# Kernel optimization log

Measured on AMD Instinct MI355X. Metric: run time of the kernel, lower is better.

## Reference

```python
import jax, jax.numpy as jnp
import numpy as np

B, S, V, E = 64, 100, 20000, 128
U, I = 10000, 20000


def setup_inputs() -> dict:
    key = jax.random.key(0)
    ks = jax.random.split(key, 12)
    initrange = 0.1
    return {
        "attr_item": jax.random.randint(ks[0], (B, S), 0, V, dtype=jnp.int32),
        "attr_tf_item": jax.random.uniform(ks[1], (B, S), dtype=jnp.float32),
        "attr_lens_item": jax.random.randint(ks[2], (B,), 1, S + 1, dtype=jnp.int32),
        "item_ids": jax.random.randint(ks[3], (B,), 0, I, dtype=jnp.int32),
        "attr_user": jax.random.randint(ks[4], (B, S), 0, V, dtype=jnp.int32),
        "attr_tf_user": jax.random.uniform(ks[5], (B, S), dtype=jnp.float32),
        "attr_lens_user": jax.random.randint(ks[6], (B,), 1, S + 1, dtype=jnp.int32),
        "user_ids": jax.random.randint(ks[7], (B,), 0, U, dtype=jnp.int32),
        "W_item": jax.random.uniform(ks[8], (V, E), jnp.float32, -initrange, initrange),
        "W_user": jax.random.uniform(ks[9], (V, E), jnp.float32, -initrange, initrange),
        "user_emb": jax.random.uniform(ks[10], (U, E), jnp.float32, -initrange, initrange),
        "item_emb": jax.random.uniform(ks[11], (I, E), jnp.float32, -initrange, initrange),
    }


def _cluster_logits(attr_ids, attr_tf, attr_lens, W):
    # attr_ids: [B,S] int, attr_tf: [B,S] float, attr_lens: [B] int, W: [V,E]
    seq = attr_ids.shape[1]
    mask = (jnp.arange(seq)[None, :] < attr_lens[:, None]).astype(attr_tf.dtype)  # [B,S]
    emb = W[attr_ids]                                   # [B,S,E]
    scores = jnp.einsum("bse,ve->bsv", emb, W)          # [B,S,V]
    cw = jax.nn.softmax(scores, axis=1)                 # softmax over seq dim (dim=1 in torch)
    # Algebraically identical to the [B,S,V,E] broadcast-mul-sum in the original:
    # logits[b,v] = sum_s (tf*mask)[b,s] * cw[b,s,v] * scores[b,s,v]
    return jnp.einsum("bs,bsv,bsv->bv", attr_tf * mask, cw, scores)


def reference(attr_item, attr_tf_item, attr_lens_item, item_ids,
              attr_user, attr_tf_user, attr_lens_user, user_ids,
              W_item, W_user, user_emb, item_emb):
    logits = _cluster_logits(attr_item, attr_tf_item, attr_lens_item, W_item)
    logits = logits + _cluster_logits(attr_user, attr_tf_user, attr_lens_user, W_user)
    logits = logits + user_emb[user_ids] @ W_user.T     # [B,V]
    logits = logits + item_emb[item_ids] @ W_item.T     # [B,V]
    return logits
```

## Files before the change

kernel.cpp:

```cpp
#include <hip/hip_runtime.h>

#define VDIM 20000
#define EDIM 128
#define BATCH 64
#define SEQ 100

typedef float f32x4 __attribute__((ext_vector_type(4)));
typedef short bf16x8 __attribute__((ext_vector_type(8)));
typedef unsigned short ushortx8 __attribute__((ext_vector_type(8)));

typedef __attribute__((address_space(1))) const unsigned int gas_u32;
typedef __attribute__((address_space(3))) unsigned int las_u32;

__device__ __forceinline__ void async16(unsigned short* lds, const unsigned short* g) {
  __builtin_amdgcn_global_load_lds((gas_u32*)g, (las_u32*)lds, 16, 0, 0);
}

__device__ __forceinline__ unsigned short f2bf(float f) {
  unsigned u = __builtin_bit_cast(unsigned, f);
  u += 0x7FFFu + ((u >> 16) & 1u);
  return (unsigned short)(u >> 16);
}

__global__ void prep_kernel(const float* __restrict__ Wi, const float* __restrict__ Wu,
                            const int* __restrict__ attr_item, const int* __restrict__ attr_user,
                            const int* __restrict__ item_ids, const int* __restrict__ user_ids,
                            const float* __restrict__ item_emb, const float* __restrict__ user_emb,
                            unsigned short* __restrict__ wbf, unsigned short* __restrict__ abf) {
  const int bid = blockIdx.x, t = threadIdx.x;
  if (bid < 2500) {
    const int c = bid & 1;
    const float* src = c ? Wu : Wi;
    unsigned short* dst = wbf + (size_t)c * (VDIM * EDIM);
    const int i0 = ((bid >> 1) * 256 + t) * 8;
    float4 a = *(const float4*)(src + i0);
    float4 b = *(const float4*)(src + i0 + 4);
    ushortx8 o;
    o[0] = f2bf(a.x); o[1] = f2bf(a.y); o[2] = f2bf(a.z); o[3] = f2bf(a.w);
    o[4] = f2bf(b.x); o[5] = f2bf(b.y); o[6] = f2bf(b.z); o[7] = f2bf(b.w);
    *(ushortx8*)(dst + i0) = o;
  } else {
    const int g = bid - 2500;
    const int b = g & 63, c = g >> 6;
    const int r = t >> 1, h = t & 1;
    const int* ids = c ? attr_user : attr_item;
    const float* W = c ? Wu : Wi;
    const float* demb = c ? user_emb : item_emb;
    const int* dids = c ? user_ids : item_ids;
    unsigned short* dst = abf + (size_t)(c * BATCH + b) * 16384;
    const float* src = nullptr;
    if (r < SEQ)       src = W + (size_t)ids[b * SEQ + r] * EDIM;
    else if (r == SEQ) src = demb + (size_t)dids[b] * EDIM;
    if (src) {
      #pragma unroll
      for (int k = 0; k < 8; ++k) {
        const int jj = h * 8 + k;
        const int j = jj ^ (r & 15);
        float4 a  = *(const float4*)(src + j * 8);
        float4 bb = *(const float4*)(src + j * 8 + 4);
        ushortx8 o;
        o[0] = f2bf(a.x);  o[1] = f2bf(a.y);  o[2] = f2bf(a.z);  o[3] = f2bf(a.w);
        o[4] = f2bf(bb.x); o[5] = f2bf(bb.y); o[6] = f2bf(bb.z); o[7] = f2bf(bb.w);
        *(ushortx8*)(dst + (r * 16 + jj) * 8) = o;
      }
    } else {
      ushortx8 z = {0, 0, 0, 0, 0, 0, 0, 0};
      #pragma unroll
      for (int k = 0; k < 8; ++k) *(ushortx8*)(dst + (r * 16 + h * 8 + k) * 8) = z;
    }
  }
}

__global__ __launch_bounds__(256, 2)
void main_kernel(const unsigned short* __restrict__ wbf, const unsigned short* __restrict__ abf,
                 const float* __restrict__ tf_item, const int* __restrict__ lens_item,
                 const float* __restrict__ tf_user, const int* __restrict__ lens_user,
                 float* __restrict__ out) {
  __shared__ __align__(16) unsigned short sA[2][16384];
  __shared__ float sDen[2][2][128];
  __shared__ float sNum[2][2][128];
  __shared__ float sDir[2][128];
  __shared__ float sTF[2][4][128];
  __shared__ int   sLen[2][4];
  __shared__ float sRes[4][128];

  const int t = threadIdx.x;
  const int v0 = blockIdx.x * 128;
  const int bg4 = blockIdx.y * 4;
  const int lane = t & 63, wave = t >> 6;
  const int wm = wave >> 1, wn = wave & 1;
  const int quad = lane >> 4, l15 = lane & 15;

  for (int k = t; k < 800; k += 256) {
    const int c = k / 400, r2 = k - c * 400;
    const int bi = r2 / 100, si = r2 - bi * 100;
    sTF[c][bi][si] = (c ? tf_user : tf_item)[(bg4 + bi) * SEQ + si];
  }
  if (t < 8) sLen[t >> 2][t & 3] = ((t >= 4) ? lens_user : lens_item)[bg4 + (t & 3)];

  bf16x8 breg[4][4];
  #pragma unroll
  for (int nt = 0; nt < 4; ++nt) {
    const int v = v0 + wn * 64 + nt * 16 + l15;
    const unsigned short* p = wbf + (size_t)v * EDIM + quad * 8;
    const bool ok = (v < VDIM);
    #pragma unroll
    for (int ks = 0; ks < 4; ++ks) {
      bf16x8 z = {0, 0, 0, 0, 0, 0, 0, 0};
      breg[nt][ks] = ok ? *(const bf16x8*)(p + ks * 32) : z;
    }
  }

  {
    const unsigned short* gb = abf + (size_t)bg4 * 16384;
    #pragma unroll
    for (int i = 0; i < 8; ++i)
      async16(&sA[0][(i * 256 + wave * 64) * 8], gb + (size_t)(i * 256 + t) * 8);
  }

  #pragma unroll 1
  for (int s = 0; s < 8; ++s) {
    const int c = s >> 2, it = s & 3, buf = s & 1;

    __syncthreads();

    if (s < 7) {
      const int ns = s + 1;
      const unsigned short* gb = abf + (size_t)((ns >> 2) * BATCH + bg4 + (ns & 3)) * 16384;
      #pragma unroll
      for (int i = 0; i < 8; ++i)
        async16(&sA[buf ^ 1][(i * 256 + wave * 64) * 8], gb + (size_t)(i * 256 + t) * 8);
    }

    if (s > 0 && t < 128) {
      const int ps = s - 1, p = ps & 1, pit = ps & 3;
      float den = sDen[p][0][t] + sDen[p][1][t];
      float num = sNum[p][0][t] + sNum[p][1][t];
      float dir = sDir[p][t];
      den -= 27.f + __expf(dir);
      const float val = num / den + dir;
      if (ps < 4) sRes[pit][t] = val;
      else {
        const int v = v0 + t;
        if (v < VDIM) out[(size_t)(bg4 + pit) * VDIM + v] = sRes[pit][t] + val;
      }
    }

    f32x4 acc[4][4];
    #pragma unroll
    for (int mt = 0; mt < 4; ++mt)
      #pragma unroll
      for (int nt = 0; nt < 4; ++nt) { f32x4 z = {0.f, 0.f, 0.f, 0.f}; acc[mt][nt] = z; }

    const unsigned char* pA = (const unsigned char*)&sA[buf][0];
    #pragma unroll
    for (int ks = 0; ks < 4; ++ks) {
      const int j = ks * 4 + quad;
      const int sw = ((j ^ l15) << 4);
      bf16x8 af[4];
      #pragma unroll
      for (int mt = 0; mt < 4; ++mt)
        af[mt] = *(const bf16x8*)(pA + (wm * 64 + mt * 16 + l15) * 256 + sw);
      #pragma unroll
      for (int mt = 0; mt < 4; ++mt)
        #pragma unroll
        for (int nt = 0; nt < 4; ++nt)
          acc[mt][nt] = __builtin_amdgcn_mfma_f32_16x16x32_bf16(af[mt], breg[nt][ks], acc[mt][nt], 0, 0, 0);
    }

    if (s == 3) {
      const unsigned short* wb1 = wbf + (size_t)VDIM * EDIM;
      #pragma unroll
      for (int nt = 0; nt < 4; ++nt) {
        const int v = v0 + wn * 64 + nt * 16 + l15;
        const unsigned short* p = wb1 + (size_t)v * EDIM + quad * 8;
        const bool ok = (v < VDIM);
        #pragma unroll
        for (int ks = 0; ks < 4; ++ks) {
          bf16x8 z = {0, 0, 0, 0, 0, 0, 0, 0};
          breg[nt][ks] = ok ? *(const bf16x8*)(p + ks * 32) : z;
        }
      }
    }

    const int lenb = sLen[c][it];
    float wv[4][4];
    #pragma unroll
    for (int mt = 0; mt < 4; ++mt)
      #pragma unroll
      for (int r = 0; r < 4; ++r) {
        const int row = wm * 64 + mt * 16 + quad * 4 + r;
        wv[mt][r] = (row < lenb) ? sTF[c][it][row] : 0.f;
      }

    #pragma unroll
    for (int nt = 0; nt < 4; ++nt) {
      float den = 0.f, num = 0.f;
      #pragma unroll
      for (int mt = 0; mt < 4; ++mt)
        #pragma unroll
        for (int r = 0; r < 4; ++r) {
          const float v = acc[mt][nt][r];
          const float e = __expf(v);
          den += e;
          num = fmaf(wv[mt][r], e * v, num);
        }
      den += __shfl_xor(den, 16, 64);
      den += __shfl_xor(den, 32, 64);
      num += __shfl_xor(num, 16, 64);
      num += __shfl_xor(num, 32, 64);
      const int col = wn * 64 + nt * 16 + l15;
      if (quad == 0) {
        sDen[buf][wm][col] = den;
        sNum[buf][wm][col] = num;
      }
      if (wm == 1 && quad == 1) sDir[buf][col] = acc[2][nt][0];
    }
  }

  __syncthreads();

  if (t < 128) {
    float den = sDen[1][0][t] + sDen[1][1][t];
    float num = sNum[1][0][t] + sNum[1][1][t];
    float dir = sDir[1][t];
    den -= 27.f + __expf(dir);
    const float val = num / den + dir;
    const int v = v0 + t;
    if (v < VDIM) out[(size_t)(bg4 + 3) * VDIM + v] = sRes[3][t] + val;
  }
}

extern "C" void kernel_launch(void* const* d_in, const int* in_sizes, int n_in,
                              void* d_out, int out_size, void* d_ws, size_t ws_size,
                              hipStream_t stream) {
  const int*   attr_item = (const int*)d_in[0];
  const float* tf_item   = (const float*)d_in[1];
  const int*   lens_item = (const int*)d_in[2];
  const int*   item_ids  = (const int*)d_in[3];
  const int*   attr_user = (const int*)d_in[4];
  const float* tf_user   = (const float*)d_in[5];
  const int*   lens_user = (const int*)d_in[6];
  const int*   user_ids  = (const int*)d_in[7];
  const float* W_item    = (const float*)d_in[8];
  const float* W_user    = (const float*)d_in[9];
  const float* user_emb  = (const float*)d_in[10];
  const float* item_emb  = (const float*)d_in[11];
  float* out = (float*)d_out;

  unsigned short* wbf = (unsigned short*)d_ws;
  unsigned short* abf = wbf + (size_t)2 * VDIM * EDIM;

  prep_kernel<<<dim3(2500 + 128), 256, 0, stream>>>(W_item, W_user, attr_item, attr_user,
                                                    item_ids, user_ids, item_emb, user_emb,
                                                    wbf, abf);
  main_kernel<<<dim3(157, 16), 256, 0, stream>>>(wbf, abf, tf_item, lens_item,
                                                 tf_user, lens_user, out);
}
```

Baseline: 252.4 us.

## Split main kernel into 512-thread blocks with 64-column tiles and 8 waves

The main kernel now uses 512 threads (8 waves) per block over a 128-row by 64-column tile instead of 256 threads over a 128 by 128 tile. The grid is transposed so that batch groups vary fastest. Each wave holds a smaller 2x2 accumulator set, which lowers register pressure and raises occupancy. The padding-row correction changes from subtracting 27 plus exp(dir) to masking rows at or beyond SEQ in the last row group. In exchange, each block reloads the A tiles for only half as many columns, so A traffic per output doubles, and a fourth partial reduction is added.

```diff
diff --git a/kernel.cpp b/kernel.cpp
--- a/kernel.cpp
+++ b/kernel.cpp
@@ -71,37 +71,39 @@
   }
 }
 
-__global__ __launch_bounds__(256, 2)
+__global__ __launch_bounds__(512, 4)
 void main_kernel(const unsigned short* __restrict__ wbf, const unsigned short* __restrict__ abf,
                  const float* __restrict__ tf_item, const int* __restrict__ lens_item,
                  const float* __restrict__ tf_user, const int* __restrict__ lens_user,
                  float* __restrict__ out) {
   __shared__ __align__(16) unsigned short sA[2][16384];
-  __shared__ float sDen[2][2][128];
-  __shared__ float sNum[2][2][128];
-  __shared__ float sDir[2][128];
-  __shared__ float sTF[2][4][128];
+  __shared__ float sDen[2][4][64];
+  __shared__ float sNum[2][4][64];
+  __shared__ float sDir[2][64];
+  __shared__ float sTF[2][4][104];
   __shared__ int   sLen[2][4];
-  __shared__ float sRes[4][128];
+  __shared__ float sRes[4][64];
 
   const int t = threadIdx.x;
-  const int v0 = blockIdx.x * 128;
-  const int bg4 = blockIdx.y * 4;
+  const int bg4 = blockIdx.x * 4;
+  const int v0 = blockIdx.y * 64;
   const int lane = t & 63, wave = t >> 6;
   const int wm = wave >> 1, wn = wave & 1;
   const int quad = lane >> 4, l15 = lane & 15;
 
-  for (int k = t; k < 800; k += 256) {
-    const int c = k / 400, r2 = k - c * 400;
-    const int bi = r2 / 100, si = r2 - bi * 100;
-    sTF[c][bi][si] = (c ? tf_user : tf_item)[(bg4 + bi) * SEQ + si];
+  for (int k = t; k < 832; k += 512) {
+    const int c = k / 416, rem = k - c * 416;
+    const int bi = rem / 104, si = rem - bi * 104;
+    float w = 0.f;
+    if (si < SEQ) w = (c ? tf_user : tf_item)[(bg4 + bi) * SEQ + si];
+    sTF[c][bi][si] = w;
   }
   if (t < 8) sLen[t >> 2][t & 3] = ((t >= 4) ? lens_user : lens_item)[bg4 + (t & 3)];
 
-  bf16x8 breg[4][4];
+  bf16x8 breg[2][4];
   #pragma unroll
-  for (int nt = 0; nt < 4; ++nt) {
-    const int v = v0 + wn * 64 + nt * 16 + l15;
+  for (int nt = 0; nt < 2; ++nt) {
+    const int v = v0 + wn * 32 + nt * 16 + l15;
     const unsigned short* p = wbf + (size_t)v * EDIM + quad * 8;
     const bool ok = (v < VDIM);
     #pragma unroll
@@ -114,8 +116,8 @@
   {
     const unsigned short* gb = abf + (size_t)bg4 * 16384;
     #pragma unroll
-    for (int i = 0; i < 8; ++i)
-      async16(&sA[0][(i * 256 + wave * 64) * 8], gb + (size_t)(i * 256 + t) * 8);
+    for (int i = 0; i < 4; ++i)
+      async16(&sA[0][(i * 512 + wave * 64) * 8], gb + (size_t)(i * 512 + t) * 8);
   }
 
   #pragma unroll 1
@@ -128,17 +130,15 @@
       const int ns = s + 1;
       const unsigned short* gb = abf + (size_t)((ns >> 2) * BATCH + bg4 + (ns & 3)) * 16384;
       #pragma unroll
-      for (int i = 0; i < 8; ++i)
-        async16(&sA[buf ^ 1][(i * 256 + wave * 64) * 8], gb + (size_t)(i * 256 + t) * 8);
-    }
-
-    if (s > 0 && t < 128) {
+      for (int i = 0; i < 4; ++i)
+        async16(&sA[buf ^ 1][(i * 512 + wave * 64) * 8], gb + (size_t)(i * 512 + t) * 8);
+    }
+
+    if (s > 0 && t < 64) {
       const int ps = s - 1, p = ps & 1, pit = ps & 3;
-      float den = sDen[p][0][t] + sDen[p][1][t];
-      float num = sNum[p][0][t] + sNum[p][1][t];
-      float dir = sDir[p][t];
-      den -= 27.f + __expf(dir);
-      const float val = num / den + dir;
+      float den = sDen[p][0][t] + sDen[p][1][t] + sDen[p][2][t] + sDen[p][3][t];
+      float num = sNum[p][0][t] + sNum[p][1][t] + sNum[p][2][t] + sNum[p][3][t];
+      const float val = num / den + sDir[p][t];
       if (ps < 4) sRes[pit][t] = val;
       else {
         const int v = v0 + t;
@@ -146,33 +146,33 @@
       }
     }
 
-    f32x4 acc[4][4];
-    #pragma unroll
-    for (int mt = 0; mt < 4; ++mt)
-      #pragma unroll
-      for (int nt = 0; nt < 4; ++nt) { f32x4 z = {0.f, 0.f, 0.f, 0.f}; acc[mt][nt] = z; }
+    f32x4 acc[2][2];
+    #pragma unroll
+    for (int mt = 0; mt < 2; ++mt)
+      #pragma unroll
+      for (int nt = 0; nt < 2; ++nt) { f32x4 z = {0.f, 0.f, 0.f, 0.f}; acc[mt][nt] = z; }
 
     const unsigned char* pA = (const unsigned char*)&sA[buf][0];
     #pragma unroll
     for (int ks = 0; ks < 4; ++ks) {
       const int j = ks * 4 + quad;
       const int sw = ((j ^ l15) << 4);
-      bf16x8 af[4];
-      #pragma unroll
-      for (int mt = 0; mt < 4; ++mt)
-        af[mt] = *(const bf16x8*)(pA + (wm * 64 + mt * 16 + l15) * 256 + sw);
-      #pragma unroll
-      for (int mt = 0; mt < 4; ++mt)
-        #pragma unroll
-        for (int nt = 0; nt < 4; ++nt)
+      bf16x8 af[2];
+      #pragma unroll
+      for (int mt = 0; mt < 2; ++mt)
+        af[mt] = *(const bf16x8*)(pA + (wm * 32 + mt * 16 + l15) * 256 + sw);
+      #pragma unroll
+      for (int mt = 0; mt < 2; ++mt)
+        #pragma unroll
+        for (int nt = 0; nt < 2; ++nt)
           acc[mt][nt] = __builtin_amdgcn_mfma_f32_16x16x32_bf16(af[mt], breg[nt][ks], acc[mt][nt], 0, 0, 0);
     }
 
     if (s == 3) {
       const unsigned short* wb1 = wbf + (size_t)VDIM * EDIM;
       #pragma unroll
-      for (int nt = 0; nt < 4; ++nt) {
-        const int v = v0 + wn * 64 + nt * 16 + l15;
+      for (int nt = 0; nt < 2; ++nt) {
+        const int v = v0 + wn * 32 + nt * 16 + l15;
         const unsigned short* p = wb1 + (size_t)v * EDIM + quad * 8;
         const bool ok = (v < VDIM);
         #pragma unroll
@@ -184,48 +184,72 @@
     }
 
     const int lenb = sLen[c][it];
-    float wv[4][4];
-    #pragma unroll
-    for (int mt = 0; mt < 4; ++mt)
-      #pragma unroll
-      for (int r = 0; r < 4; ++r) {
-        const int row = wm * 64 + mt * 16 + quad * 4 + r;
-        wv[mt][r] = (row < lenb) ? sTF[c][it][row] : 0.f;
-      }
-
-    #pragma unroll
-    for (int nt = 0; nt < 4; ++nt) {
-      float den = 0.f, num = 0.f;
-      #pragma unroll
-      for (int mt = 0; mt < 4; ++mt)
+    if (wm < 3) {
+      float wv[2][4];
+      #pragma unroll
+      for (int mt = 0; mt < 2; ++mt)
         #pragma unroll
         for (int r = 0; r < 4; ++r) {
-          const float v = acc[mt][nt][r];
+          const int row = wm * 32 + mt * 16 + quad * 4 + r;
+          wv[mt][r] = (row < lenb) ? sTF[c][it][row] : 0.f;
+        }
+      #pragma unroll
+      for (int nt = 0; nt < 2; ++nt) {
+        float den = 0.f, num = 0.f;
+        #pragma unroll
+        for (int mt = 0; mt < 2; ++mt)
+          #pragma unroll
+          for (int r = 0; r < 4; ++r) {
+            const float v = acc[mt][nt][r];
+            const float e = __expf(v);
+            den += e;
+            num = fmaf(wv[mt][r], e * v, num);
+          }
+        den += __shfl_xor(den, 16, 64);
+        den += __shfl_xor(den, 32, 64);
+        num += __shfl_xor(num, 16, 64);
+        num += __shfl_xor(num, 32, 64);
+        const int col = wn * 32 + nt * 16 + l15;
+        if (quad == 0) {
+          sDen[buf][wm][col] = den;
+          sNum[buf][wm][col] = num;
+        }
+      }
+    } else {
+      #pragma unroll
+      for (int nt = 0; nt < 2; ++nt) {
+        float den = 0.f, num = 0.f;
+        #pragma unroll
+        for (int r = 0; r < 4; ++r) {
+          const int row = 96 + quad * 4 + r;
+          const float v = acc[0][nt][r];
           const float e = __expf(v);
-          den += e;
-          num = fmaf(wv[mt][r], e * v, num);
-        }
-      den += __shfl_xor(den, 16, 64);
-      den += __shfl_xor(den, 32, 64);
-      num += __shfl_xor(num, 16, 64);
-      num += __shfl_xor(num, 32, 64);
-      const int col = wn * 64 + nt * 16 + l15;
-      if (quad == 0) {
-        sDen[buf][wm][col] = den;
-        sNum[buf][wm][col] = num;
-      }
-      if (wm == 1 && quad == 1) sDir[buf][col] = acc[2][nt][0];
+          const bool real = (row < SEQ);
+          den += real ? e : 0.f;
+          const int idx = row < 104 ? row : 103;
+          const float w = (row < lenb) ? sTF[c][it][idx] : 0.f;
+          num = fmaf(w, real ? e * v : 0.f, num);
+        }
+        den += __shfl_xor(den, 16, 64);
+        den += __shfl_xor(den, 32, 64);
+        num += __shfl_xor(num, 16, 64);
+        num += __shfl_xor(num, 32, 64);
+        const int col = wn * 32 + nt * 16 + l15;
+        if (quad == 0) {
+          sDen[buf][3][col] = den;
+          sNum[buf][3][col] = num;
+        }
+        if (quad == 1) sDir[buf][col] = acc[0][nt][0];
+      }
     }
   }
 
   __syncthreads();
 
-  if (t < 128) {
-    float den = sDen[1][0][t] + sDen[1][1][t];
-    float num = sNum[1][0][t] + sNum[1][1][t];
-    float dir = sDir[1][t];
-    den -= 27.f + __expf(dir);
-    const float val = num / den + dir;
+  if (t < 64) {
+    float den = sDen[1][0][t] + sDen[1][1][t] + sDen[1][2][t] + sDen[1][3][t];
+    float num = sNum[1][0][t] + sNum[1][1][t] + sNum[1][2][t] + sNum[1][3][t];
+    const float val = num / den + sDir[1][t];
     const int v = v0 + t;
     if (v < VDIM) out[(size_t)(bg4 + 3) * VDIM + v] = sRes[3][t] + val;
   }
@@ -254,6 +278,6 @@
   prep_kernel<<<dim3(2500 + 128), 256, 0, stream>>>(W_item, W_user, attr_item, attr_user,
                                                     item_ids, user_ids, item_emb, user_emb,
                                                     wbf, abf);
-  main_kernel<<<dim3(157, 16), 256, 0, stream>>>(wbf, abf, tf_item, lens_item,
+  main_kernel<<<dim3(16, 313), 512, 0, stream>>>(wbf, abf, tf_item, lens_item,
                                                  tf_user, lens_user, out);
 }
```

Result: slower. 308.4 us (+22.2%).

## Shrink vocab tile to 96, single-buffer LDS, raise occupancy to three blocks

Applied to the files above, without the earlier changes.

Reduces the per-block vocabulary tile from 128 to 96 columns, so each wave holds 3 instead of 4 B fragments. The A tile drops from double to single buffering, with an extra barrier and the next prefetch issued after the MFMA loop. Together these aim for 3 blocks per CU instead of 2 and a grid of 209x16 blocks. It also skips the padded M tile in the softmax reduction for the second wave row (the padding-correction constant changes from 27 to 11 to match) and swaps the division for a hardware reciprocal. Dropping double buffering exposes global load latency that must now be hidden by the extra occupancy.

```diff
diff --git a/kernel.cpp b/kernel.cpp
--- a/kernel.cpp
+++ b/kernel.cpp
@@ -4,6 +4,8 @@
 #define EDIM 128
 #define BATCH 64
 #define SEQ 100
+#define BN 96
+#define NVT 209
 
 typedef float f32x4 __attribute__((ext_vector_type(4)));
 typedef short bf16x8 __attribute__((ext_vector_type(8)));
@@ -71,37 +73,39 @@
   }
 }
 
-__global__ __launch_bounds__(256, 2)
+__global__ __launch_bounds__(256, 3)
 void main_kernel(const unsigned short* __restrict__ wbf, const unsigned short* __restrict__ abf,
                  const float* __restrict__ tf_item, const int* __restrict__ lens_item,
                  const float* __restrict__ tf_user, const int* __restrict__ lens_user,
                  float* __restrict__ out) {
-  __shared__ __align__(16) unsigned short sA[2][16384];
-  __shared__ float sDen[2][2][128];
-  __shared__ float sNum[2][2][128];
-  __shared__ float sDir[2][128];
+  __shared__ __align__(16) unsigned short sA[16384];
+  __shared__ float sDen[2][2][BN];
+  __shared__ float sNum[2][2][BN];
+  __shared__ float sDir[2][BN];
   __shared__ float sTF[2][4][128];
   __shared__ int   sLen[2][4];
-  __shared__ float sRes[4][128];
+  __shared__ float sRes[4][BN];
 
   const int t = threadIdx.x;
-  const int v0 = blockIdx.x * 128;
+  const int v0 = blockIdx.x * BN;
   const int bg4 = blockIdx.y * 4;
   const int lane = t & 63, wave = t >> 6;
   const int wm = wave >> 1, wn = wave & 1;
   const int quad = lane >> 4, l15 = lane & 15;
 
-  for (int k = t; k < 800; k += 256) {
-    const int c = k / 400, r2 = k - c * 400;
-    const int bi = r2 / 100, si = r2 - bi * 100;
-    sTF[c][bi][si] = (c ? tf_user : tf_item)[(bg4 + bi) * SEQ + si];
+  #pragma unroll
+  for (int k = t; k < 1024; k += 256) {
+    const int c = k >> 9, bi = (k >> 7) & 3, si = k & 127;
+    float w = 0.f;
+    if (si < SEQ) w = (c ? tf_user : tf_item)[(bg4 + bi) * SEQ + si];
+    sTF[c][bi][si] = w;
   }
   if (t < 8) sLen[t >> 2][t & 3] = ((t >= 4) ? lens_user : lens_item)[bg4 + (t & 3)];
 
-  bf16x8 breg[4][4];
+  bf16x8 breg[3][4];
   #pragma unroll
-  for (int nt = 0; nt < 4; ++nt) {
-    const int v = v0 + wn * 64 + nt * 16 + l15;
+  for (int nt = 0; nt < 3; ++nt) {
+    const int v = v0 + wn * 48 + nt * 16 + l15;
     const unsigned short* p = wbf + (size_t)v * EDIM + quad * 8;
     const bool ok = (v < VDIM);
     #pragma unroll
@@ -115,7 +119,7 @@
     const unsigned short* gb = abf + (size_t)bg4 * 16384;
     #pragma unroll
     for (int i = 0; i < 8; ++i)
-      async16(&sA[0][(i * 256 + wave * 64) * 8], gb + (size_t)(i * 256 + t) * 8);
+      async16(&sA[(i * 256 + wave * 64) * 8], gb + (size_t)(i * 256 + t) * 8);
   }
 
   #pragma unroll 1
@@ -124,21 +128,13 @@
 
     __syncthreads();
 
-    if (s < 7) {
-      const int ns = s + 1;
-      const unsigned short* gb = abf + (size_t)((ns >> 2) * BATCH + bg4 + (ns & 3)) * 16384;
-      #pragma unroll
-      for (int i = 0; i < 8; ++i)
-        async16(&sA[buf ^ 1][(i * 256 + wave * 64) * 8], gb + (size_t)(i * 256 + t) * 8);
-    }
-
-    if (s > 0 && t < 128) {
+    if (s > 0 && t < BN) {
       const int ps = s - 1, p = ps & 1, pit = ps & 3;
       float den = sDen[p][0][t] + sDen[p][1][t];
       float num = sNum[p][0][t] + sNum[p][1][t];
-      float dir = sDir[p][t];
-      den -= 27.f + __expf(dir);
-      const float val = num / den + dir;
+      const float dir = sDir[p][t];
+      den -= 11.f + __expf(dir);
+      const float val = num * __builtin_amdgcn_rcpf(den) + dir;
       if (ps < 4) sRes[pit][t] = val;
       else {
         const int v = v0 + t;
@@ -146,13 +142,13 @@
       }
     }
 
-    f32x4 acc[4][4];
+    f32x4 acc[4][3];
     #pragma unroll
     for (int mt = 0; mt < 4; ++mt)
       #pragma unroll
-      for (int nt = 0; nt < 4; ++nt) { f32x4 z = {0.f, 0.f, 0.f, 0.f}; acc[mt][nt] = z; }
-
-    const unsigned char* pA = (const unsigned char*)&sA[buf][0];
+      for (int nt = 0; nt < 3; ++nt) { f32x4 z = {0.f, 0.f, 0.f, 0.f}; acc[mt][nt] = z; }
+
+    const unsigned char* pA = (const unsigned char*)&sA[0];
     #pragma unroll
     for (int ks = 0; ks < 4; ++ks) {
       const int j = ks * 4 + quad;
@@ -164,15 +160,24 @@
       #pragma unroll
       for (int mt = 0; mt < 4; ++mt)
         #pragma unroll
-        for (int nt = 0; nt < 4; ++nt)
+        for (int nt = 0; nt < 3; ++nt)
           acc[mt][nt] = __builtin_amdgcn_mfma_f32_16x16x32_bf16(af[mt], breg[nt][ks], acc[mt][nt], 0, 0, 0);
     }
 
+    __syncthreads();
+
+    if (s < 7) {
+      const int ns = s + 1;
+      const unsigned short* gb = abf + (size_t)((ns >> 2) * BATCH + bg4 + (ns & 3)) * 16384;
+      #pragma unroll
+      for (int i = 0; i < 8; ++i)
+        async16(&sA[(i * 256 + wave * 64) * 8], gb + (size_t)(i * 256 + t) * 8);
+    }
     if (s == 3) {
       const unsigned short* wb1 = wbf + (size_t)VDIM * EDIM;
       #pragma unroll
-      for (int nt = 0; nt < 4; ++nt) {
-        const int v = v0 + wn * 64 + nt * 16 + l15;
+      for (int nt = 0; nt < 3; ++nt) {
+        const int v = v0 + wn * 48 + nt * 16 + l15;
         const unsigned short* p = wb1 + (size_t)v * EDIM + quad * 8;
         const bool ok = (v < VDIM);
         #pragma unroll
@@ -184,20 +189,20 @@
     }
 
     const int lenb = sLen[c][it];
+    const int mtend = (wm == 0) ? 4 : 3;
     float wv[4][4];
     #pragma unroll
     for (int mt = 0; mt < 4; ++mt)
       #pragma unroll
       for (int r = 0; r < 4; ++r) {
         const int row = wm * 64 + mt * 16 + quad * 4 + r;
-        wv[mt][r] = (row < lenb) ? sTF[c][it][row] : 0.f;
-      }
-
-    #pragma unroll
-    for (int nt = 0; nt < 4; ++nt) {
+        wv[mt][r] = (row < lenb) ? sTF[c][it][row & 127] : 0.f;
+      }
+
+    #pragma unroll
+    for (int nt = 0; nt < 3; ++nt) {
       float den = 0.f, num = 0.f;
-      #pragma unroll
-      for (int mt = 0; mt < 4; ++mt)
+      for (int mt = 0; mt < mtend; ++mt)
         #pragma unroll
         for (int r = 0; r < 4; ++r) {
           const float v = acc[mt][nt][r];
@@ -209,7 +214,7 @@
       den += __shfl_xor(den, 32, 64);
       num += __shfl_xor(num, 16, 64);
       num += __shfl_xor(num, 32, 64);
-      const int col = wn * 64 + nt * 16 + l15;
+      const int col = wn * 48 + nt * 16 + l15;
       if (quad == 0) {
         sDen[buf][wm][col] = den;
         sNum[buf][wm][col] = num;
@@ -220,12 +225,12 @@
 
   __syncthreads();
 
-  if (t < 128) {
+  if (t < BN) {
     float den = sDen[1][0][t] + sDen[1][1][t];
     float num = sNum[1][0][t] + sNum[1][1][t];
-    float dir = sDir[1][t];
-    den -= 27.f + __expf(dir);
-    const float val = num / den + dir;
+    const float dir = sDir[1][t];
+    den -= 11.f + __expf(dir);
+    const float val = num * __builtin_amdgcn_rcpf(den) + dir;
     const int v = v0 + t;
     if (v < VDIM) out[(size_t)(bg4 + 3) * VDIM + v] = sRes[3][t] + val;
   }
@@ -254,6 +259,6 @@
   prep_kernel<<<dim3(2500 + 128), 256, 0, stream>>>(W_item, W_user, attr_item, attr_user,
                                                     item_ids, user_ids, item_emb, user_emb,
                                                     wbf, abf);
-  main_kernel<<<dim3(157, 16), 256, 0, stream>>>(wbf, abf, tf_item, lens_item,
+  main_kernel<<<dim3(NVT, 16), 256, 0, stream>>>(wbf, abf, tf_item, lens_item,
                                                  tf_user, lens_user, out);
 }
```

After: 521.5 us. +106.6%, slower.
